# Kernel optimization log

Hardware: AMD Instinct MI355X
Metric: run time of the kernel (lower is better)

## Reference

```python
import jax, jax.numpy as jnp
import numpy as np

SEQ, BATCH, IN_DIM, NQ = 512, 512, 128, 8  # hidden_dim == n_qubits == 8


def setup_inputs() -> dict:
    key = jax.random.key(0)
    k1, k2, k3, k4 = jax.random.split(key, 4)
    inputs = jax.random.normal(k1, (SEQ, BATCH, IN_DIM), dtype=jnp.float32)
    h0 = jnp.zeros((BATCH, NQ), dtype=jnp.float32)
    c0 = jnp.zeros((BATCH, NQ), dtype=jnp.float32)
    D = IN_DIM + NQ
    # gate order: forget, input, update, output
    W = jax.random.normal(k2, (4, NQ, D), dtype=jnp.float32) / np.sqrt(D)
    b = jnp.zeros((4, NQ), dtype=jnp.float32)
    qp = jax.random.normal(k3, (4, NQ), dtype=jnp.float32)  # QLayer.params per gate
    return {"inputs": inputs, "h0": h0, "c0": c0, "W": W, "b": b, "qp": qp}


def _qlayer(z):
    # Analytic form of the RY/RY/CNOT-chain circuit: <Z_k> = prod_{j<=k} cos(theta_j)
    return jnp.cumprod(jnp.cos(z), axis=-1)


def reference(inputs, h0, c0, W, b, qp):
    def step(carry, x_t):
        h, c = carry
        comb = jnp.concatenate([x_t, h], axis=-1)            # (B, D)
        z = jnp.einsum('bd,gqd->bgq', comb, W) + b + qp      # (B, 4, NQ)
        q = _qlayer(z)
        f = jax.nn.sigmoid(q[:, 0])
        i = jax.nn.sigmoid(q[:, 1])
        g = jnp.tanh(q[:, 2])
        o = jax.nn.sigmoid(q[:, 3])
        c2 = f * c + i * g
        h2 = o * jnp.tanh(c2)
        return (h2, c2), h2

    (h_f, c_f), outputs = jax.lax.scan(step, (h0, c0), inputs)
    return outputs, h_f, c_f
```

## Files before the change

### kernel.cpp

```cpp
#include <hip/hip_runtime.h>


#define SEQ_LEN 512
#define BATCH_N 512
#define IN_DIMC 128
#define DTOT 136
#define OUT_MAIN (SEQ_LEN * BATCH_N * 8)

__global__ __launch_bounds__(256) void zx_gemm(
    const float* __restrict__ X, const float* __restrict__ W,
    const float* __restrict__ bv, const float* __restrict__ qp,
    float* __restrict__ ZX)
{
    __shared__ __align__(16) float Wl[IN_DIMC * 32];
    const int tid = threadIdx.x;
    #pragma unroll
    for (int i = 0; i < 16; ++i) {
        int idx = i * 256 + tid;
        Wl[idx] = W[(idx & 31) * DTOT + (idx >> 5)];
    }
    __syncthreads();

    const long r0 = (long)blockIdx.x * 512 + tid;
    const long r1 = r0 + 256;
    const float4* __restrict__ X40 = (const float4*)X + r0 * 32;
    const float4* __restrict__ X41 = (const float4*)X + r1 * 32;
    const float4* __restrict__ W4  = (const float4*)Wl;

    float4 a0[8], a1[8];
    #pragma unroll
    for (int qq = 0; qq < 8; ++qq) {
        a0[qq] = make_float4(0.f, 0.f, 0.f, 0.f);
        a1[qq] = make_float4(0.f, 0.f, 0.f, 0.f);
    }

    float4 xa = X40[0], xb = X41[0];
    #pragma unroll 1
    for (int k4 = 0; k4 < 32; ++k4) {
        float4 xan = xa, xbn = xb;
        if (k4 < 31) { xan = X40[k4 + 1]; xbn = X41[k4 + 1]; }
        #pragma unroll
        for (int c = 0; c < 4; ++c) {
            const float va = (c==0)?xa.x:(c==1)?xa.y:(c==2)?xa.z:xa.w;
            const float vb = (c==0)?xb.x:(c==1)?xb.y:(c==2)?xb.z:xb.w;
            #pragma unroll
            for (int qq = 0; qq < 8; ++qq) {
                const float4 w = W4[(k4 * 4 + c) * 8 + qq];
                a0[qq].x = fmaf(va, w.x, a0[qq].x);
                a0[qq].y = fmaf(va, w.y, a0[qq].y);
                a0[qq].z = fmaf(va, w.z, a0[qq].z);
                a0[qq].w = fmaf(va, w.w, a0[qq].w);
                a1[qq].x = fmaf(vb, w.x, a1[qq].x);
                a1[qq].y = fmaf(vb, w.y, a1[qq].y);
                a1[qq].z = fmaf(vb, w.z, a1[qq].z);
                a1[qq].w = fmaf(vb, w.w, a1[qq].w);
            }
        }
        xa = xan; xb = xbn;
    }

    float4* __restrict__ Z4 = (float4*)ZX;
    #pragma unroll
    for (int qq = 0; qq < 8; ++qq) {
        const int g0 = qq * 4;
        float4 o0 = a0[qq], o1 = a1[qq];
        const float b0 = bv[g0+0] + qp[g0+0];
        const float b1_ = bv[g0+1] + qp[g0+1];
        const float b2 = bv[g0+2] + qp[g0+2];
        const float b3 = bv[g0+3] + qp[g0+3];
        o0.x += b0; o0.y += b1_; o0.z += b2; o0.w += b3;
        o1.x += b0; o1.y += b1_; o1.z += b2; o1.w += b3;
        Z4[r0 * 8 + qq] = o0;
        Z4[r1 * 8 + qq] = o1;
    }
}

#define DPP_F(x, ctrl) \
    __builtin_bit_cast(float, __builtin_amdgcn_update_dpp( \
        0, __builtin_bit_cast(int, (x)), (ctrl), 0xF, 0xF, true))

__global__ __launch_bounds__(64) void qlstm_scan(
    const float* __restrict__ ZX, const float* __restrict__ W,
    const float* __restrict__ h0, const float* __restrict__ c0,
    float* __restrict__ out)
{
    const int l   = threadIdx.x;
    const int l16 = l & 15;
    const int q   = l & 7;
    const int hB  = l16 >> 3;
    const int row = blockIdx.x * 4 + (l >> 4);
    const int gq0 = l16;
    const int gq1 = 16 + l16;

    const float qf = (float)q;
    int jmap[8];
    jmap[0] = q;
    jmap[1] = (int)DPP_F(qf, 0x121);
    jmap[2] = (int)DPP_F(qf, 0x122);
    jmap[3] = (int)DPP_F(qf, 0x123);
    jmap[4] = (int)DPP_F(qf, 0x124);
    jmap[5] = (int)DPP_F(qf, 0x125);
    jmap[6] = (int)DPP_F(qf, 0x126);
    jmap[7] = (int)DPP_F(qf, 0x127);

    const bool dirshr = ((int)DPP_F(qf, 0x111) == q - 1);

    float wh0[8], wh1[8], hror[8];
    #pragma unroll
    for (int r = 0; r < 8; ++r) {
        wh0[r]  = W[gq0 * DTOT + IN_DIMC + jmap[r]];
        wh1[r]  = W[gq1 * DTOT + IN_DIMC + jmap[r]];
        hror[r] = h0[row * 8 + jmap[r]];
    }
    float c = c0[row * 8 + q];

    const bool ge1 = (q >= 1), ge2 = (q >= 2), ge4 = (q >= 4);
    const bool isT = (hB == 0);
    const float m1 = isT ? -2.f : -1.f;
    const float A1 = isT ?  2.f :  1.f;
    const float B1 = isT ? -1.f :  0.f;

    float zb0  = ZX[(long)row * 32 + l16];
    float zb1  = ZX[(long)row * 32 + 16 + l16];
    float zn10 = ZX[((long)BATCH_N + row) * 32 + l16];
    float zn11 = ZX[((long)BATCH_N + row) * 32 + 16 + l16];

    float hlast = 0.f;
    for (int t = 0; t < SEQ_LEN; ++t) {
        const long tp = (t + 2 < SEQ_LEN) ? (t + 2) : (SEQ_LEN - 1);
        const float zn20 = ZX[(tp * BATCH_N + row) * 32 + l16];
        const float zn21 = ZX[(tp * BATCH_N + row) * 32 + 16 + l16];

        float s0a = fmaf(hror[0], wh0[0], zb0);
        s0a = fmaf(hror[1], wh0[1], s0a);
        s0a = fmaf(hror[2], wh0[2], s0a);
        s0a = fmaf(hror[3], wh0[3], s0a);
        float s0b = hror[4] * wh0[4];
        s0b = fmaf(hror[5], wh0[5], s0b);
        s0b = fmaf(hror[6], wh0[6], s0b);
        s0b = fmaf(hror[7], wh0[7], s0b);
        const float z0 = s0a + s0b;

        float s1a = fmaf(hror[0], wh1[0], zb1);
        s1a = fmaf(hror[1], wh1[1], s1a);
        s1a = fmaf(hror[2], wh1[2], s1a);
        s1a = fmaf(hror[3], wh1[3], s1a);
        float s1b = hror[4] * wh1[4];
        s1b = fmaf(hror[5], wh1[5], s1b);
        s1b = fmaf(hror[6], wh1[6], s1b);
        s1b = fmaf(hror[7], wh1[7], s1b);
        const float z1 = s1a + s1b;

        float p0 = __cosf(z0), p1 = __cosf(z1);

        float ashr = p0, ashl = p0, bshr = p1, bshl = p1;
        { float v = DPP_F(ashr, 0x111); ashr *= ge1 ? v : 1.f; }
        { float v = DPP_F(bshr, 0x111); bshr *= ge1 ? v : 1.f; }
        { float v = DPP_F(ashl, 0x101); ashl *= ge1 ? v : 1.f; }
        { float v = DPP_F(bshl, 0x101); bshl *= ge1 ? v : 1.f; }
        { float v = DPP_F(ashr, 0x112); ashr *= ge2 ? v : 1.f; }
        { float v = DPP_F(bshr, 0x112); bshr *= ge2 ? v : 1.f; }
        { float v = DPP_F(ashl, 0x102); ashl *= ge2 ? v : 1.f; }
        { float v = DPP_F(bshl, 0x102); bshl *= ge2 ? v : 1.f; }
        { float v = DPP_F(ashr, 0x114); ashr *= ge4 ? v : 1.f; }
        { float v = DPP_F(bshr, 0x114); bshr *= ge4 ? v : 1.f; }
        { float v = DPP_F(ashl, 0x104); ashl *= ge4 ? v : 1.f; }
        { float v = DPP_F(bshl, 0x104); bshl *= ge4 ? v : 1.f; }
        p0 = dirshr ? ashr : ashl;
        p1 = dirshr ? bshr : bshl;

        const float act0 = __builtin_amdgcn_rcpf(1.f + __expf(-p0));
        const float act1 = fmaf(
            __builtin_amdgcn_rcpf(1.f + __expf(p1 * m1)), A1, B1);

        const float oth0 = DPP_F(act0, 0x128);
        const float oth1 = DPP_F(act1, 0x128);

        const float f_ = hB ? oth0 : act0;
        const float i_ = hB ? act0 : oth0;
        const float g_ = hB ? oth1 : act1;
        const float o_ = hB ? act1 : oth1;

        const float c2 = fmaf(f_, c, i_ * g_);
        const float th = fmaf(
            __builtin_amdgcn_rcpf(1.f + __expf(-2.f * c2)), 2.f, -1.f);
        const float h2 = o_ * th;
        c = c2;
        hlast = h2;

        if (l16 < 8) out[((long)t * BATCH_N + row) * 8 + q] = h2;

        hror[0] = h2;
        hror[1] = DPP_F(h2, 0x121);
        hror[2] = DPP_F(h2, 0x122);
        hror[3] = DPP_F(h2, 0x123);
        hror[4] = DPP_F(h2, 0x124);
        hror[5] = DPP_F(h2, 0x125);
        hror[6] = DPP_F(h2, 0x126);
        hror[7] = DPP_F(h2, 0x127);

        zb0 = zn10; zb1 = zn11;
        zn10 = zn20; zn11 = zn21;
    }

    if (l16 < 8) {
        out[OUT_MAIN + row * 8 + q] = hlast;
        out[OUT_MAIN + BATCH_N * 8 + row * 8 + q] = c;
    }
}

extern "C" void kernel_launch(void* const* d_in, const int* in_sizes, int n_in,
                              void* d_out, int out_size, void* d_ws, size_t ws_size,
                              hipStream_t stream)
{
    const float* X  = (const float*)d_in[0];
    const float* h0 = (const float*)d_in[1];
    const float* c0 = (const float*)d_in[2];
    const float* W  = (const float*)d_in[3];
    const float* bv = (const float*)d_in[4];
    const float* qp = (const float*)d_in[5];
    float* out = (float*)d_out;
    float* ZX  = (float*)d_ws;

    zx_gemm<<<(SEQ_LEN * BATCH_N) / 512, 256, 0, stream>>>(X, W, bv, qp, ZX);
    qlstm_scan<<<BATCH_N / 4, 64, 0, stream>>>(ZX, W, h0, c0, out);
}
```

Baseline: 389.6 us.

## Approximate gate activations with polynomials, widen GEMM rows, deepen prefetch, uniform DPP branch

The gate sigmoid and tanh, whose inputs are cumulative cosine products in [-1,1], now use low-degree odd polynomials instead of exp and reciprocal. The cumprod direction select becomes a wave-uniform branch, so only one DPP chain runs. The ZX prefetch deepens to three steps, and h2 uses exp2 with a folded fma. The input GEMM computes four rows per thread in half as many blocks with launch bounds of one block, which raises register pressure and lowers parallelism. The polynomial approximations add small numerical error that holds only on the bounded range.

```diff
diff --git a/kernel.cpp b/kernel.cpp
--- a/kernel.cpp
+++ b/kernel.cpp
@@ -7,7 +7,7 @@
 #define DTOT 136
 #define OUT_MAIN (SEQ_LEN * BATCH_N * 8)
 
-__global__ __launch_bounds__(256) void zx_gemm(
+__global__ __launch_bounds__(256, 1) void zx_gemm(
     const float* __restrict__ X, const float* __restrict__ W,
     const float* __restrict__ bv, const float* __restrict__ qp,
     float* __restrict__ ZX)
@@ -21,28 +21,37 @@
     }
     __syncthreads();
 
-    const long r0 = (long)blockIdx.x * 512 + tid;
-    const long r1 = r0 + 256;
-    const float4* __restrict__ X40 = (const float4*)X + r0 * 32;
-    const float4* __restrict__ X41 = (const float4*)X + r1 * 32;
-    const float4* __restrict__ W4  = (const float4*)Wl;
-
-    float4 a0[8], a1[8];
+    const long r0 = (long)blockIdx.x * 1024 + tid;
+    const long r1 = r0 + 256, r2 = r0 + 512, r3 = r0 + 768;
+    const float4* __restrict__ X0 = (const float4*)X + r0 * 32;
+    const float4* __restrict__ X1 = (const float4*)X + r1 * 32;
+    const float4* __restrict__ X2 = (const float4*)X + r2 * 32;
+    const float4* __restrict__ X3 = (const float4*)X + r3 * 32;
+    const float4* __restrict__ W4 = (const float4*)Wl;
+
+    float4 a0[8], a1[8], a2[8], a3[8];
     #pragma unroll
     for (int qq = 0; qq < 8; ++qq) {
         a0[qq] = make_float4(0.f, 0.f, 0.f, 0.f);
         a1[qq] = make_float4(0.f, 0.f, 0.f, 0.f);
-    }
-
-    float4 xa = X40[0], xb = X41[0];
+        a2[qq] = make_float4(0.f, 0.f, 0.f, 0.f);
+        a3[qq] = make_float4(0.f, 0.f, 0.f, 0.f);
+    }
+
+    float4 xa = X0[0], xb = X1[0], xc = X2[0], xd = X3[0];
     #pragma unroll 1
     for (int k4 = 0; k4 < 32; ++k4) {
-        float4 xan = xa, xbn = xb;
-        if (k4 < 31) { xan = X40[k4 + 1]; xbn = X41[k4 + 1]; }
+        float4 xan = xa, xbn = xb, xcn = xc, xdn = xd;
+        if (k4 < 31) {
+            xan = X0[k4 + 1]; xbn = X1[k4 + 1];
+            xcn = X2[k4 + 1]; xdn = X3[k4 + 1];
+        }
         #pragma unroll
         for (int c = 0; c < 4; ++c) {
             const float va = (c==0)?xa.x:(c==1)?xa.y:(c==2)?xa.z:xa.w;
             const float vb = (c==0)?xb.x:(c==1)?xb.y:(c==2)?xb.z:xb.w;
+            const float vc = (c==0)?xc.x:(c==1)?xc.y:(c==2)?xc.z:xc.w;
+            const float vd = (c==0)?xd.x:(c==1)?xd.y:(c==2)?xd.z:xd.w;
             #pragma unroll
             for (int qq = 0; qq < 8; ++qq) {
                 const float4 w = W4[(k4 * 4 + c) * 8 + qq];
@@ -54,30 +63,51 @@
                 a1[qq].y = fmaf(vb, w.y, a1[qq].y);
                 a1[qq].z = fmaf(vb, w.z, a1[qq].z);
                 a1[qq].w = fmaf(vb, w.w, a1[qq].w);
+                a2[qq].x = fmaf(vc, w.x, a2[qq].x);
+                a2[qq].y = fmaf(vc, w.y, a2[qq].y);
+                a2[qq].z = fmaf(vc, w.z, a2[qq].z);
+                a2[qq].w = fmaf(vc, w.w, a2[qq].w);
+                a3[qq].x = fmaf(vd, w.x, a3[qq].x);
+                a3[qq].y = fmaf(vd, w.y, a3[qq].y);
+                a3[qq].z = fmaf(vd, w.z, a3[qq].z);
+                a3[qq].w = fmaf(vd, w.w, a3[qq].w);
             }
         }
-        xa = xan; xb = xbn;
+        xa = xan; xb = xbn; xc = xcn; xd = xdn;
     }
 
     float4* __restrict__ Z4 = (float4*)ZX;
     #pragma unroll
     for (int qq = 0; qq < 8; ++qq) {
         const int g0 = qq * 4;
-        float4 o0 = a0[qq], o1 = a1[qq];
         const float b0 = bv[g0+0] + qp[g0+0];
         const float b1_ = bv[g0+1] + qp[g0+1];
         const float b2 = bv[g0+2] + qp[g0+2];
         const float b3 = bv[g0+3] + qp[g0+3];
+        float4 o0 = a0[qq], o1 = a1[qq], o2 = a2[qq], o3 = a3[qq];
         o0.x += b0; o0.y += b1_; o0.z += b2; o0.w += b3;
         o1.x += b0; o1.y += b1_; o1.z += b2; o1.w += b3;
+        o2.x += b0; o2.y += b1_; o2.z += b2; o2.w += b3;
+        o3.x += b0; o3.y += b1_; o3.z += b2; o3.w += b3;
         Z4[r0 * 8 + qq] = o0;
         Z4[r1 * 8 + qq] = o1;
+        Z4[r2 * 8 + qq] = o2;
+        Z4[r3 * 8 + qq] = o3;
     }
 }
 
 #define DPP_F(x, ctrl) \
     __builtin_bit_cast(float, __builtin_amdgcn_update_dpp( \
         0, __builtin_bit_cast(int, (x)), (ctrl), 0xF, 0xF, true))
+
+#define SIG_A0 0.25f
+#define SIG_A1 (-0.020833333f)
+#define SIG_A2 0.0020833333f
+#define TNH_T0 0.999752f
+#define TNH_T1 (-0.329199f)
+#define TNH_T2 0.115682f
+#define TNH_T3 (-0.024641f)
+#define NL2E2 (-2.8853900817779268f)
 
 __global__ __launch_bounds__(64) void qlstm_scan(
     const float* __restrict__ ZX, const float* __restrict__ W,
@@ -103,7 +133,8 @@
     jmap[6] = (int)DPP_F(qf, 0x126);
     jmap[7] = (int)DPP_F(qf, 0x127);
 
-    const bool dirshr = ((int)DPP_F(qf, 0x111) == q - 1);
+    const int dircal = ((int)DPP_F(qf, 0x111) == q - 1) ? 1 : 0;
+    const int dirU = __builtin_amdgcn_readlane(dircal, 1);
 
     float wh0[8], wh1[8], hror[8];
     #pragma unroll
@@ -116,20 +147,19 @@
 
     const bool ge1 = (q >= 1), ge2 = (q >= 2), ge4 = (q >= 4);
     const bool isT = (hB == 0);
-    const float m1 = isT ? -2.f : -1.f;
-    const float A1 = isT ?  2.f :  1.f;
-    const float B1 = isT ? -1.f :  0.f;
 
     float zb0  = ZX[(long)row * 32 + l16];
     float zb1  = ZX[(long)row * 32 + 16 + l16];
-    float zn10 = ZX[((long)BATCH_N + row) * 32 + l16];
-    float zn11 = ZX[((long)BATCH_N + row) * 32 + 16 + l16];
+    float zn10 = ZX[((long)1 * BATCH_N + row) * 32 + l16];
+    float zn11 = ZX[((long)1 * BATCH_N + row) * 32 + 16 + l16];
+    float zn20 = ZX[((long)2 * BATCH_N + row) * 32 + l16];
+    float zn21 = ZX[((long)2 * BATCH_N + row) * 32 + 16 + l16];
 
     float hlast = 0.f;
     for (int t = 0; t < SEQ_LEN; ++t) {
-        const long tp = (t + 2 < SEQ_LEN) ? (t + 2) : (SEQ_LEN - 1);
-        const float zn20 = ZX[(tp * BATCH_N + row) * 32 + l16];
-        const float zn21 = ZX[(tp * BATCH_N + row) * 32 + 16 + l16];
+        const long tp = (t + 3 < SEQ_LEN) ? (t + 3) : (SEQ_LEN - 1);
+        const float zn30 = ZX[(tp * BATCH_N + row) * 32 + l16];
+        const float zn31 = ZX[(tp * BATCH_N + row) * 32 + 16 + l16];
 
         float s0a = fmaf(hror[0], wh0[0], zb0);
         s0a = fmaf(hror[1], wh0[1], s0a);
@@ -153,25 +183,32 @@
 
         float p0 = __cosf(z0), p1 = __cosf(z1);
 
-        float ashr = p0, ashl = p0, bshr = p1, bshl = p1;
-        { float v = DPP_F(ashr, 0x111); ashr *= ge1 ? v : 1.f; }
-        { float v = DPP_F(bshr, 0x111); bshr *= ge1 ? v : 1.f; }
-        { float v = DPP_F(ashl, 0x101); ashl *= ge1 ? v : 1.f; }
-        { float v = DPP_F(bshl, 0x101); bshl *= ge1 ? v : 1.f; }
-        { float v = DPP_F(ashr, 0x112); ashr *= ge2 ? v : 1.f; }
-        { float v = DPP_F(bshr, 0x112); bshr *= ge2 ? v : 1.f; }
-        { float v = DPP_F(ashl, 0x102); ashl *= ge2 ? v : 1.f; }
-        { float v = DPP_F(bshl, 0x102); bshl *= ge2 ? v : 1.f; }
-        { float v = DPP_F(ashr, 0x114); ashr *= ge4 ? v : 1.f; }
-        { float v = DPP_F(bshr, 0x114); bshr *= ge4 ? v : 1.f; }
-        { float v = DPP_F(ashl, 0x104); ashl *= ge4 ? v : 1.f; }
-        { float v = DPP_F(bshl, 0x104); bshl *= ge4 ? v : 1.f; }
-        p0 = dirshr ? ashr : ashl;
-        p1 = dirshr ? bshr : bshl;
-
-        const float act0 = __builtin_amdgcn_rcpf(1.f + __expf(-p0));
-        const float act1 = fmaf(
-            __builtin_amdgcn_rcpf(1.f + __expf(p1 * m1)), A1, B1);
+        if (dirU) {
+            { float v = DPP_F(p0, 0x111); p0 *= ge1 ? v : 1.f; }
+            { float v = DPP_F(p1, 0x111); p1 *= ge1 ? v : 1.f; }
+            { float v = DPP_F(p0, 0x112); p0 *= ge2 ? v : 1.f; }
+            { float v = DPP_F(p1, 0x112); p1 *= ge2 ? v : 1.f; }
+            { float v = DPP_F(p0, 0x114); p0 *= ge4 ? v : 1.f; }
+            { float v = DPP_F(p1, 0x114); p1 *= ge4 ? v : 1.f; }
+        } else {
+            { float v = DPP_F(p0, 0x101); p0 *= ge1 ? v : 1.f; }
+            { float v = DPP_F(p1, 0x101); p1 *= ge1 ? v : 1.f; }
+            { float v = DPP_F(p0, 0x102); p0 *= ge2 ? v : 1.f; }
+            { float v = DPP_F(p1, 0x102); p1 *= ge2 ? v : 1.f; }
+            { float v = DPP_F(p0, 0x104); p0 *= ge4 ? v : 1.f; }
+            { float v = DPP_F(p1, 0x104); p1 *= ge4 ? v : 1.f; }
+        }
+
+        const float y0 = p0 * p0;
+        const float P0 = fmaf(y0, fmaf(y0, SIG_A2, SIG_A1), SIG_A0);
+        const float act0 = fmaf(p0, P0, 0.5f);
+
+        const float y1 = p1 * p1;
+        const float P1s = fmaf(y1, fmaf(y1, SIG_A2, SIG_A1), SIG_A0);
+        const float sg1 = fmaf(p1, P1s, 0.5f);
+        const float P1t = fmaf(y1, fmaf(y1, fmaf(y1, TNH_T3, TNH_T2), TNH_T1), TNH_T0);
+        const float th1 = p1 * P1t;
+        const float act1 = isT ? th1 : sg1;
 
         const float oth0 = DPP_F(act0, 0x128);
         const float oth1 = DPP_F(act1, 0x128);
@@ -182,9 +219,10 @@
         const float o_ = hB ? act1 : oth1;
 
         const float c2 = fmaf(f_, c, i_ * g_);
-        const float th = fmaf(
-            __builtin_amdgcn_rcpf(1.f + __expf(-2.f * c2)), 2.f, -1.f);
-        const float h2 = o_ * th;
+        const float r_ = __builtin_amdgcn_rcpf(
+            1.f + __builtin_amdgcn_exp2f(c2 * NL2E2));
+        const float o2_ = o_ + o_;
+        const float h2 = fmaf(r_, o2_, -o_);
         c = c2;
         hlast = h2;
 
@@ -201,6 +239,7 @@
 
         zb0 = zn10; zb1 = zn11;
         zn10 = zn20; zn11 = zn21;
+        zn20 = zn30; zn21 = zn31;
     }
 
     if (l16 < 8) {
@@ -222,6 +261,6 @@
     float* out = (float*)d_out;
     float* ZX  = (float*)d_ws;
 
-    zx_gemm<<<(SEQ_LEN * BATCH_N) / 512, 256, 0, stream>>>(X, W, bv, qp, ZX);
+    zx_gemm<<<(SEQ_LEN * BATCH_N) / 1024, 256, 0, stream>>>(X, W, bv, qp, ZX);
     qlstm_scan<<<BATCH_N / 4, 64, 0, stream>>>(ZX, W, h0, c0, out);
 }
```

Result: no change. 396.8 us (+1.9%).

## Interleave four batch rows per wavefront and use polynomial gate activations

Applied to the files above, without the earlier changes.

Each 64-lane wavefront now carries four independent recurrence chains (NS=4), so the latency of each serial step can be hidden by work from the other chains. The ZX prefetch depth grows to four steps. The shift direction of the DPP scan is now resolved once, uniformly across the wavefront, instead of computing both directions every step. Sigmoid and tanh of the cumprod values, which lie in [-1,1], are replaced by low-order polynomials, and the cell tanh uses exp2. The launch drops to 32 blocks of 64 threads, which uses far fewer CUs, and the polynomials introduce approximation error.

```diff
diff --git a/kernel.cpp b/kernel.cpp
--- a/kernel.cpp
+++ b/kernel.cpp
@@ -6,6 +6,7 @@
 #define IN_DIMC 128
 #define DTOT 136
 #define OUT_MAIN (SEQ_LEN * BATCH_N * 8)
+#define NS 4
 
 __global__ __launch_bounds__(256) void zx_gemm(
     const float* __restrict__ X, const float* __restrict__ W,
@@ -79,6 +80,15 @@
     __builtin_bit_cast(float, __builtin_amdgcn_update_dpp( \
         0, __builtin_bit_cast(int, (x)), (ctrl), 0xF, 0xF, true))
 
+#define SIG_A0 0.25f
+#define SIG_A1 (-0.020833333f)
+#define SIG_A2 0.0020833333f
+#define TNH_T0 0.999752f
+#define TNH_T1 (-0.329199f)
+#define TNH_T2 0.115682f
+#define TNH_T3 (-0.024641f)
+#define NL2E2 (-2.8853900817779268f)
+
 __global__ __launch_bounds__(64) void qlstm_scan(
     const float* __restrict__ ZX, const float* __restrict__ W,
     const float* __restrict__ h0, const float* __restrict__ c0,
@@ -88,7 +98,7 @@
     const int l16 = l & 15;
     const int q   = l & 7;
     const int hB  = l16 >> 3;
-    const int row = blockIdx.x * 4 + (l >> 4);
+    const int rb  = blockIdx.x * 16 + (l >> 4);
     const int gq0 = l16;
     const int gq1 = 16 + l16;
 
@@ -103,109 +113,164 @@
     jmap[6] = (int)DPP_F(qf, 0x126);
     jmap[7] = (int)DPP_F(qf, 0x127);
 
-    const bool dirshr = ((int)DPP_F(qf, 0x111) == q - 1);
-
-    float wh0[8], wh1[8], hror[8];
+    const int dircal = ((int)DPP_F(qf, 0x111) == q - 1) ? 1 : 0;
+    const int dirU = __builtin_amdgcn_readlane(dircal, 1);
+
+    float wh0[8], wh1[8];
     #pragma unroll
     for (int r = 0; r < 8; ++r) {
-        wh0[r]  = W[gq0 * DTOT + IN_DIMC + jmap[r]];
-        wh1[r]  = W[gq1 * DTOT + IN_DIMC + jmap[r]];
-        hror[r] = h0[row * 8 + jmap[r]];
-    }
-    float c = c0[row * 8 + q];
+        wh0[r] = W[gq0 * DTOT + IN_DIMC + jmap[r]];
+        wh1[r] = W[gq1 * DTOT + IN_DIMC + jmap[r]];
+    }
+
+    float hror[NS][8], c[NS], hlast[NS];
+    #pragma unroll
+    for (int s = 0; s < NS; ++s) {
+        const int row = rb + 4 * s;
+        #pragma unroll
+        for (int r = 0; r < 8; ++r) hror[s][r] = h0[row * 8 + jmap[r]];
+        c[s] = c0[row * 8 + q];
+        hlast[s] = 0.f;
+    }
 
     const bool ge1 = (q >= 1), ge2 = (q >= 2), ge4 = (q >= 4);
     const bool isT = (hB == 0);
-    const float m1 = isT ? -2.f : -1.f;
-    const float A1 = isT ?  2.f :  1.f;
-    const float B1 = isT ? -1.f :  0.f;
-
-    float zb0  = ZX[(long)row * 32 + l16];
-    float zb1  = ZX[(long)row * 32 + 16 + l16];
-    float zn10 = ZX[((long)BATCH_N + row) * 32 + l16];
-    float zn11 = ZX[((long)BATCH_N + row) * 32 + 16 + l16];
-
-    float hlast = 0.f;
-    for (int t = 0; t < SEQ_LEN; ++t) {
-        const long tp = (t + 2 < SEQ_LEN) ? (t + 2) : (SEQ_LEN - 1);
-        const float zn20 = ZX[(tp * BATCH_N + row) * 32 + l16];
-        const float zn21 = ZX[(tp * BATCH_N + row) * 32 + 16 + l16];
-
-        float s0a = fmaf(hror[0], wh0[0], zb0);
-        s0a = fmaf(hror[1], wh0[1], s0a);
-        s0a = fmaf(hror[2], wh0[2], s0a);
-        s0a = fmaf(hror[3], wh0[3], s0a);
-        float s0b = hror[4] * wh0[4];
-        s0b = fmaf(hror[5], wh0[5], s0b);
-        s0b = fmaf(hror[6], wh0[6], s0b);
-        s0b = fmaf(hror[7], wh0[7], s0b);
-        const float z0 = s0a + s0b;
-
-        float s1a = fmaf(hror[0], wh1[0], zb1);
-        s1a = fmaf(hror[1], wh1[1], s1a);
-        s1a = fmaf(hror[2], wh1[2], s1a);
-        s1a = fmaf(hror[3], wh1[3], s1a);
-        float s1b = hror[4] * wh1[4];
-        s1b = fmaf(hror[5], wh1[5], s1b);
-        s1b = fmaf(hror[6], wh1[6], s1b);
-        s1b = fmaf(hror[7], wh1[7], s1b);
-        const float z1 = s1a + s1b;
-
-        float p0 = __cosf(z0), p1 = __cosf(z1);
-
-        float ashr = p0, ashl = p0, bshr = p1, bshl = p1;
-        { float v = DPP_F(ashr, 0x111); ashr *= ge1 ? v : 1.f; }
-        { float v = DPP_F(bshr, 0x111); bshr *= ge1 ? v : 1.f; }
-        { float v = DPP_F(ashl, 0x101); ashl *= ge1 ? v : 1.f; }
-        { float v = DPP_F(bshl, 0x101); bshl *= ge1 ? v : 1.f; }
-        { float v = DPP_F(ashr, 0x112); ashr *= ge2 ? v : 1.f; }
-        { float v = DPP_F(bshr, 0x112); bshr *= ge2 ? v : 1.f; }
-        { float v = DPP_F(ashl, 0x102); ashl *= ge2 ? v : 1.f; }
-        { float v = DPP_F(bshl, 0x102); bshl *= ge2 ? v : 1.f; }
-        { float v = DPP_F(ashr, 0x114); ashr *= ge4 ? v : 1.f; }
-        { float v = DPP_F(bshr, 0x114); bshr *= ge4 ? v : 1.f; }
-        { float v = DPP_F(ashl, 0x104); ashl *= ge4 ? v : 1.f; }
-        { float v = DPP_F(bshl, 0x104); bshl *= ge4 ? v : 1.f; }
-        p0 = dirshr ? ashr : ashl;
-        p1 = dirshr ? bshr : bshl;
-
-        const float act0 = __builtin_amdgcn_rcpf(1.f + __expf(-p0));
-        const float act1 = fmaf(
-            __builtin_amdgcn_rcpf(1.f + __expf(p1 * m1)), A1, B1);
-
-        const float oth0 = DPP_F(act0, 0x128);
-        const float oth1 = DPP_F(act1, 0x128);
-
-        const float f_ = hB ? oth0 : act0;
-        const float i_ = hB ? act0 : oth0;
-        const float g_ = hB ? oth1 : act1;
-        const float o_ = hB ? act1 : oth1;
-
-        const float c2 = fmaf(f_, c, i_ * g_);
-        const float th = fmaf(
-            __builtin_amdgcn_rcpf(1.f + __expf(-2.f * c2)), 2.f, -1.f);
-        const float h2 = o_ * th;
-        c = c2;
-        hlast = h2;
-
-        if (l16 < 8) out[((long)t * BATCH_N + row) * 8 + q] = h2;
-
-        hror[0] = h2;
-        hror[1] = DPP_F(h2, 0x121);
-        hror[2] = DPP_F(h2, 0x122);
-        hror[3] = DPP_F(h2, 0x123);
-        hror[4] = DPP_F(h2, 0x124);
-        hror[5] = DPP_F(h2, 0x125);
-        hror[6] = DPP_F(h2, 0x126);
-        hror[7] = DPP_F(h2, 0x127);
-
-        zb0 = zn10; zb1 = zn11;
-        zn10 = zn20; zn11 = zn21;
+
+    float zp0[4][NS], zp1[4][NS];
+    #pragma unroll
+    for (int slot = 0; slot < 4; ++slot) {
+        #pragma unroll
+        for (int s = 0; s < NS; ++s) {
+            const long row = rb + 4 * s;
+            zp0[slot][s] = ZX[((long)slot * BATCH_N + row) * 32 + l16];
+            zp1[slot][s] = ZX[((long)slot * BATCH_N + row) * 32 + 16 + l16];
+        }
+    }
+
+    for (int t4 = 0; t4 < SEQ_LEN; t4 += 4) {
+        #pragma unroll
+        for (int u = 0; u < 4; ++u) {
+            const int t = t4 + u;
+
+            float zb0[NS], zb1[NS];
+            #pragma unroll
+            for (int s = 0; s < NS; ++s) { zb0[s] = zp0[u][s]; zb1[s] = zp1[u][s]; }
+            const long tn = (t + 4 < SEQ_LEN) ? (t + 4) : (SEQ_LEN - 1);
+            #pragma unroll
+            for (int s = 0; s < NS; ++s) {
+                const long row = rb + 4 * s;
+                zp0[u][s] = ZX[(tn * BATCH_N + row) * 32 + l16];
+                zp1[u][s] = ZX[(tn * BATCH_N + row) * 32 + 16 + l16];
+            }
+
+            float p0[NS], p1[NS];
+            #pragma unroll
+            for (int s = 0; s < NS; ++s) {
+                float s0a = fmaf(hror[s][0], wh0[0], zb0[s]);
+                s0a = fmaf(hror[s][1], wh0[1], s0a);
+                s0a = fmaf(hror[s][2], wh0[2], s0a);
+                s0a = fmaf(hror[s][3], wh0[3], s0a);
+                float s0b = hror[s][4] * wh0[4];
+                s0b = fmaf(hror[s][5], wh0[5], s0b);
+                s0b = fmaf(hror[s][6], wh0[6], s0b);
+                s0b = fmaf(hror[s][7], wh0[7], s0b);
+                p0[s] = __cosf(s0a + s0b);
+
+                float s1a = fmaf(hror[s][0], wh1[0], zb1[s]);
+                s1a = fmaf(hror[s][1], wh1[1], s1a);
+                s1a = fmaf(hror[s][2], wh1[2], s1a);
+                s1a = fmaf(hror[s][3], wh1[3], s1a);
+                float s1b = hror[s][4] * wh1[4];
+                s1b = fmaf(hror[s][5], wh1[5], s1b);
+                s1b = fmaf(hror[s][6], wh1[6], s1b);
+                s1b = fmaf(hror[s][7], wh1[7], s1b);
+                p1[s] = __cosf(s1a + s1b);
+            }
+
+            if (dirU) {
+                #pragma unroll
+                for (int s = 0; s < NS; ++s) {
+                    { float v = DPP_F(p0[s], 0x111); p0[s] *= ge1 ? v : 1.f; }
+                    { float v = DPP_F(p1[s], 0x111); p1[s] *= ge1 ? v : 1.f; }
+                }
+                #pragma unroll
+                for (int s = 0; s < NS; ++s) {
+                    { float v = DPP_F(p0[s], 0x112); p0[s] *= ge2 ? v : 1.f; }
+                    { float v = DPP_F(p1[s], 0x112); p1[s] *= ge2 ? v : 1.f; }
+                }
+                #pragma unroll
+                for (int s = 0; s < NS; ++s) {
+                    { float v = DPP_F(p0[s], 0x114); p0[s] *= ge4 ? v : 1.f; }
+                    { float v = DPP_F(p1[s], 0x114); p1[s] *= ge4 ? v : 1.f; }
+                }
+            } else {
+                #pragma unroll
+                for (int s = 0; s < NS; ++s) {
+                    { float v = DPP_F(p0[s], 0x101); p0[s] *= ge1 ? v : 1.f; }
+                    { float v = DPP_F(p1[s], 0x101); p1[s] *= ge1 ? v : 1.f; }
+                }
+                #pragma unroll
+                for (int s = 0; s < NS; ++s) {
+                    { float v = DPP_F(p0[s], 0x102); p0[s] *= ge2 ? v : 1.f; }
+                    { float v = DPP_F(p1[s], 0x102); p1[s] *= ge2 ? v : 1.f; }
+                }
+                #pragma unroll
+                for (int s = 0; s < NS; ++s) {
+                    { float v = DPP_F(p0[s], 0x104); p0[s] *= ge4 ? v : 1.f; }
+                    { float v = DPP_F(p1[s], 0x104); p1[s] *= ge4 ? v : 1.f; }
+                }
+            }
+
+            #pragma unroll
+            for (int s = 0; s < NS; ++s) {
+                const float y0 = p0[s] * p0[s];
+                const float P0 = fmaf(y0, fmaf(y0, SIG_A2, SIG_A1), SIG_A0);
+                const float act0 = fmaf(p0[s], P0, 0.5f);
+
+                const float y1 = p1[s] * p1[s];
+                const float P1s = fmaf(y1, fmaf(y1, SIG_A2, SIG_A1), SIG_A0);
+                const float sg1 = fmaf(p1[s], P1s, 0.5f);
+                const float P1t = fmaf(y1, fmaf(y1, fmaf(y1, TNH_T3, TNH_T2), TNH_T1), TNH_T0);
+                const float th1 = p1[s] * P1t;
+                const float act1 = isT ? th1 : sg1;
+
+                const float oth0 = DPP_F(act0, 0x128);
+                const float oth1 = DPP_F(act1, 0x128);
+
+                const float f_ = hB ? oth0 : act0;
+                const float i_ = hB ? act0 : oth0;
+                const float g_ = hB ? oth1 : act1;
+                const float o_ = hB ? act1 : oth1;
+
+                const float c2 = fmaf(f_, c[s], i_ * g_);
+                const float r_ = __builtin_amdgcn_rcpf(
+                    1.f + __builtin_amdgcn_exp2f(c2 * NL2E2));
+                const float h2 = fmaf(r_, o_ + o_, -o_);
+                c[s] = c2;
+                hlast[s] = h2;
+
+                if (l16 < 8)
+                    out[((long)t * BATCH_N + rb + 4 * s) * 8 + q] = h2;
+
+                hror[s][0] = h2;
+                hror[s][1] = DPP_F(h2, 0x121);
+                hror[s][2] = DPP_F(h2, 0x122);
+                hror[s][3] = DPP_F(h2, 0x123);
+                hror[s][4] = DPP_F(h2, 0x124);
+                hror[s][5] = DPP_F(h2, 0x125);
+                hror[s][6] = DPP_F(h2, 0x126);
+                hror[s][7] = DPP_F(h2, 0x127);
+            }
+        }
     }
 
     if (l16 < 8) {
-        out[OUT_MAIN + row * 8 + q] = hlast;
-        out[OUT_MAIN + BATCH_N * 8 + row * 8 + q] = c;
+        #pragma unroll
+        for (int s = 0; s < NS; ++s) {
+            const int row = rb + 4 * s;
+            out[OUT_MAIN + row * 8 + q] = hlast[s];
+            out[OUT_MAIN + BATCH_N * 8 + row * 8 + q] = c[s];
+        }
     }
 }
 
@@ -223,5 +288,5 @@
     float* ZX  = (float*)d_ws;
 
     zx_gemm<<<(SEQ_LEN * BATCH_N) / 512, 256, 0, stream>>>(X, W, bv, qp, ZX);
-    qlstm_scan<<<BATCH_N / 4, 64, 0, stream>>>(ZX, W, h0, c0, out);
+    qlstm_scan<<<BATCH_N / 16, 64, 0, stream>>>(ZX, W, h0, c0, out);
 }
```

New measurement: 601.4 us. +54.4%, slower.
